# Optimization experiments

Measured on AMD Instinct MI355X. Metric: run time of the kernel, lower is better.

## Reference

```python
import jax, jax.numpy as jnp
import numpy as np

B = 4
NV = 6890           # SMPL vertex count
NF0 = 13776         # SMPL face count (before fill_back)
T = 3               # tex_size
IMG = 128           # render image size
UVH = UVW = 256     # uv image resolution
FLENGTH = 500.0
NEAR, FAR = 0.1, 25.0
CHUNK = 128         # faces per z-buffer scan step
BIG = jnp.float32(1e10)


def setup_inputs():
    key = jax.random.key(0)
    ks = jax.random.split(key, 5)
    faces0 = jax.random.randint(ks[0], (NF0, 3), 0, NV, dtype=jnp.int32)
    faces = jnp.concatenate([faces0, faces0[:, ::-1]], axis=0)  # fill_back
    cam = jnp.concatenate([0.8 + 0.2 * jax.random.uniform(ks[1], (B, 1)),
                           0.05 * jax.random.normal(ks[2], (B, 2))], axis=1)
    vertices = 0.3 * jax.random.normal(ks[3], (B, NV, 3))
    uv_imgs = jax.random.uniform(ks[4], (B, 3, UVH, UVW))
    img2uv_sampler = jax.random.uniform(jax.random.fold_in(key, 7),
                                        (faces.shape[0], T * T, 2)) * 2.0 - 1.0
    return {"cam": cam, "vertices": vertices, "uv_imgs": uv_imgs,
            "img2uv_sampler": img2uv_sampler, "faces": faces}


def _grid_sample(img, grid):
    # img (B,C,H,W), grid (B,N,2) xy in [-1,1]; bilinear, align_corners=False, zeros padding
    Bc, C, H, W = img.shape
    x = (grid[..., 0] + 1.0) * (W * 0.5) - 0.5
    y = (grid[..., 1] + 1.0) * (H * 0.5) - 0.5
    x0f = jnp.floor(x); y0f = jnp.floor(y)
    wx = x - x0f; wy = y - y0f
    x0 = x0f.astype(jnp.int32); y0 = y0f.astype(jnp.int32)
    imgf = img.reshape(Bc, C, H * W)
    def gat(yi, xi, w):
        valid = (xi >= 0) & (xi < W) & (yi >= 0) & (yi < H)
        idx = jnp.clip(yi, 0, H - 1) * W + jnp.clip(xi, 0, W - 1)
        v = jax.vmap(lambda im, i: im[:, i])(imgf, idx)  # (B,C,N)
        return v * (w * valid)[:, None, :]
    return (gat(y0, x0, (1 - wx) * (1 - wy)) + gat(y0, x0 + 1, wx * (1 - wy)) +
            gat(y0 + 1, x0, (1 - wx) * wy) + gat(y0 + 1, x0 + 1, wx * wy))


def _extract_tex(uv_imgs, sampler, nf):
    # sampler (B,nf,T*T,2) -> textures (B,nf,T,T,T,3)
    tex = _grid_sample(uv_imgs, sampler.reshape(uv_imgs.shape[0], -1, 2))
    tex = tex.reshape(-1, 3, nf, T, T).transpose(0, 2, 3, 4, 1)  # (B,nf,T,T,3)
    return jnp.broadcast_to(tex[:, :, :, :, None, :], tex.shape[:4] + (T, 3))


def _lighting(face_verts, textures):
    # module defaults: ambient intensity 1, directional 0, white lights, dir=(0,1,0)
    v0, v1, v2 = face_verts[:, :, 0], face_verts[:, :, 1], face_verts[:, :, 2]
    n = jnp.cross(v1 - v0, v2 - v0)
    n = n / (jnp.linalg.norm(n, axis=-1, keepdims=True) + 1e-10)
    cos = jnp.maximum(n @ jnp.array([0.0, 1.0, 0.0]), 0.0)       # (B,F)
    light = 1.0 * jnp.ones(3) + 0.0 * cos[..., None] * jnp.ones(3)  # (B,F,3)
    return textures * light[:, :, None, None, None, :]


def _weak_projection(cam, vertices):
    p = IMG / 2.0
    tz = FLENGTH / (p * cam[:, 0:1])                              # (B,1)
    v2d = cam[:, None, 0:1] * (vertices[:, :, :2] + cam[:, None, 1:])
    return jnp.concatenate([v2d, vertices[:, :, 2:3] + tz[:, None, :]], axis=-1)


def _bary(fv, px, py):
    # fv: (...,3,3) triangle screen verts; px,py broadcastable pixel coords
    x0 = fv[..., 0, 0]; y0 = fv[..., 0, 1]
    x1 = fv[..., 1, 0]; y1 = fv[..., 1, 1]
    x2 = fv[..., 2, 0]; y2 = fv[..., 2, 1]
    w0 = (x2 - x1) * (py - y1) - (y2 - y1) * (px - x1)
    w1 = (x0 - x2) * (py - y2) - (y0 - y2) * (px - x2)
    w2 = (x1 - x0) * (py - y0) - (y1 - y0) * (px - x0)
    area = w0 + w1 + w2
    s = jnp.where(area == 0, 1.0, area)
    return w0 / s, w1 / s, w2 / s, area


def _pixel_grid():
    xs = (2.0 * jnp.arange(IMG) + 1.0) / IMG - 1.0                # (W,)
    ys = (1.0 - (2.0 * jnp.arange(IMG) + 1.0) / IMG)[:, None]     # (H,1), +y up
    return xs, ys


def _rasterize_fim(face_verts):
    # face_verts (B,F,3,3) in screen coords -> face index map (B,H,W), -1 = bg
    Bc, F = face_verts.shape[:2]
    pad = (-F) % CHUNK
    fv = jnp.pad(face_verts, ((0, 0), (0, pad), (0, 0), (0, 0)))
    S = (F + pad) // CHUNK
    fv = fv.reshape(Bc, S, CHUNK, 3, 3).transpose(1, 0, 2, 3, 4)  # (S,B,C,3,3)
    xs, ys = _pixel_grid()
    def step(carry, inp):
        zbuf, fim = carry
        f, base = inp
        fe = f[:, :, None, None, :, :]                            # (B,C,1,1,3,3)
        b0, b1, b2, area = _bary(fe, xs, ys)                      # (B,C,H,W)
        z0 = f[:, :, 0, 2][..., None, None]
        z1 = f[:, :, 1, 2][..., None, None]
        z2 = f[:, :, 2, 2][..., None, None]
        invz = b0 / z0 + b1 / z1 + b2 / z2                        # perspective-correct
        zp = 1.0 / jnp.where(invz == 0, 1.0, invz)
        inside = (b0 >= 0) & (b1 >= 0) & (b2 >= 0) & (area > 0)   # front-facing only
        valid = inside & (zp > NEAR) & (zp < FAR)
        depth = jnp.where(valid, zp, BIG)
        dmin = jnp.min(depth, axis=1)                             # (B,H,W)
        amin = jnp.argmin(depth, axis=1).astype(jnp.int32) + base
        better = dmin < zbuf
        return (jnp.where(better, dmin, zbuf),
                jnp.where(better, amin, fim)), None
    zbuf0 = jnp.full((Bc, IMG, IMG), BIG)
    fim0 = jnp.full((Bc, IMG, IMG), -1, jnp.int32)
    bases = (jnp.arange(S) * CHUNK).astype(jnp.int32)
    (zbuf, fim), _ = jax.lax.scan(step, (zbuf0, fim0), (fv, bases))
    return fim


def _shade(face_verts, textures, fim):
    # nearest-texel barycentric texture lookup, as in neural_renderer forward
    Bc, F = face_verts.shape[:2]
    fid = jnp.clip(fim, 0, F - 1).reshape(Bc, -1)                 # (B,HW)
    fv = jax.vmap(lambda v, i: v[i])(face_verts, fid)             # (B,HW,3,3)
    fv = fv.reshape(Bc, IMG, IMG, 3, 3)
    xs, ys = _pixel_grid()
    b0, b1, b2, _ = _bary(fv, xs, ys)                             # (B,H,W)
    t0 = jnp.clip(jnp.floor(b0 * T).astype(jnp.int32), 0, T - 1)
    t1 = jnp.clip(jnp.floor(b1 * T).astype(jnp.int32), 0, T - 1)
    t2 = jnp.clip(jnp.floor(b2 * T).astype(jnp.int32), 0, T - 1)
    idx = ((jnp.clip(fim, 0, F - 1) * T + t0) * T + t1) * T + t2  # (B,H,W)
    texf = textures.reshape(Bc, F * T * T * T, 3)
    col = jax.vmap(lambda t, i: t[i])(texf, idx.reshape(Bc, -1))  # (B,HW,3)
    col = col.reshape(Bc, IMG, IMG, 3)
    col = jnp.where((fim >= 0)[..., None], col, 0.0)              # bg color (0,0,0)
    return col.transpose(0, 3, 1, 2)                              # (B,3,H,W)


def reference(cam, vertices, uv_imgs, img2uv_sampler, faces):
    Bc = cam.shape[0]
    nf = faces.shape[0]
    sampler = jnp.broadcast_to(img2uv_sampler[None], (Bc,) + img2uv_sampler.shape)
    textures = _extract_tex(uv_imgs, sampler, nf)                 # (B,nf,T,T,T,3)
    textures = _lighting(vertices[:, faces], textures)
    verts_p = _weak_projection(cam, vertices)
    fv = verts_p[:, faces]                                        # (B,nf,3,3)
    fv_sg = jax.lax.stop_gradient(fv)  # hard rasterization is non-differentiable
    fim = _rasterize_fim(fv_sg)
    images = _shade(fv_sg, textures, fim)
    return images


if __name__ == "__main__":
    out = reference(**setup_inputs())
    print(out.shape, out.dtype)
```

## Files before the change

### kernel.cpp

```cpp
#include <hip/hip_runtime.h>
#include <stdint.h>

#pragma clang fp contract(off)

#define B_    4
#define NV_   6890
#define NF_   27552
#define IMG_  128
#define UV_   256
#define NPIX  (IMG_*IMG_)

#define TS_     8
#define TPB_    (IMG_/TS_)
#define NTILE_  (TPB_*TPB_)
#define NBIN_   (B_*NTILE_)
#define NZ_     8
#define NCELL_  (NTILE_*NZ_)
#define LIST_CAP (1536*1024)
#define CAPB_   (LIST_CAP/B_)
#define MAXCB_  (CAPB_/256 + NTILE_)
#define SEEDN_  256
#define FBF_    256
#define NBLK_   ((NF_+FBF_-1)/FBF_)


__global__ void __launch_bounds__(256) project_k(
    const float* __restrict__ cam, const float* __restrict__ verts,
    float* __restrict__ vp) {
  int idx = blockIdx.x * 256 + threadIdx.x;
  if (idx >= B_ * NV_) return;
  int b = idx / NV_;
  float c0 = cam[b * 3 + 0], c1 = cam[b * 3 + 1], c2 = cam[b * 3 + 2];
  float tz = 500.0f / (64.0f * c0);
  const float* src = verts + (size_t)idx * 3;
  float* dst = vp + (size_t)idx * 4;
  dst[0] = c0 * (src[0] + c1);
  dst[1] = c0 * (src[1] + c2);
  dst[2] = src[2] + tz;
  dst[3] = 0.0f;
}

struct FaceBin {
  int valid, tx0, tx1, ty0, ty1, bu;
  float d21x, d21y, d02x, d02y, d10x, d10y;
  float x0, y0, x1, y1, x2, y2, zmin;
};

__device__ __forceinline__ FaceBin face_bin(
    const float* __restrict__ cam, const float* __restrict__ vp,
    const int* __restrict__ faces, int b, int f) {
  FaceBin r; r.valid = 0; r.zmin = 0.0f;
  int ia = faces[f * 3 + 0], ib = faces[f * 3 + 1], ic = faces[f * 3 + 2];
  const float* vb = vp + (size_t)b * NV_ * 4;
  float x0 = vb[ia * 4 + 0], y0 = vb[ia * 4 + 1], z0 = vb[ia * 4 + 2];
  float x1 = vb[ib * 4 + 0], y1 = vb[ib * 4 + 1], z1 = vb[ib * 4 + 2];
  float x2 = vb[ic * 4 + 0], y2 = vb[ic * 4 + 1], z2 = vb[ic * 4 + 2];
  float area_c = (x1 - x0) * (y2 - y0) - (y1 - y0) * (x2 - x0);
  if (area_c < -1e-3f) return r;
  float xmn = fminf(x0, fminf(x1, x2)), xmx = fmaxf(x0, fmaxf(x1, x2));
  float ymn = fminf(y0, fminf(y1, y2)), ymx = fmaxf(y0, fmaxf(y1, y2));
  int jlo = (int)floorf((xmn + 1.0f) * 64.0f - 0.5f) - 1;
  int jhi = (int)ceilf ((xmx + 1.0f) * 64.0f - 0.5f) + 1;
  int ilo = (int)floorf((1.0f - ymx) * 64.0f - 0.5f) - 1;
  int ihi = (int)ceilf ((1.0f - ymn) * 64.0f - 0.5f) + 1;
  if (jhi < 0 || ihi < 0 || jlo > IMG_ - 1 || ilo > IMG_ - 1) return r;
  jlo = max(jlo, 0); ilo = max(ilo, 0);
  jhi = min(jhi, IMG_ - 1); ihi = min(ihi, IMG_ - 1);
  r.tx0 = jlo >> 3; r.tx1 = jhi >> 3; r.ty0 = ilo >> 3; r.ty1 = ihi >> 3;
  r.zmin = fminf(z0, fminf(z1, z2));
  float tz = 500.0f / (64.0f * cam[b * 3]);
  float zr = r.zmin - tz;
  r.bu = (zr > -0.447f) + (zr > -0.367f) + (zr > -0.308f) + (zr > -0.254f) +
         (zr > -0.200f) + (zr > -0.141f) + (zr > -0.061f);
  r.d21x = x2 - x1; r.d21y = y2 - y1;
  r.d02x = x0 - x2; r.d02y = y0 - y2;
  r.d10x = x1 - x0; r.d10y = y1 - y0;
  r.x0 = x0; r.y0 = y0; r.x1 = x1; r.y1 = y1; r.x2 = x2; r.y2 = y2;
  r.valid = 1;
  return r;
}

__device__ __forceinline__ int tile_pass(const FaceBin& r, int tx, int ty) {
  float pxmin = fmaf((float)(tx * 8), 0.015625f, -0.9921875f);
  float pxmax = pxmin + 0.109375f;
  float pymax = fmaf((float)(ty * 8), -0.015625f, 0.9921875f);
  float pymin = pymax - 0.109375f;
  float w0m = r.d21x * ((r.d21x > 0.0f ? pymax : pymin) - r.y1) -
              r.d21y * ((r.d21y > 0.0f ? pxmin : pxmax) - r.x1);
  float w1m = r.d02x * ((r.d02x > 0.0f ? pymax : pymin) - r.y2) -
              r.d02y * ((r.d02y > 0.0f ? pxmin : pxmax) - r.x2);
  float w2m = r.d10x * ((r.d10x > 0.0f ? pymax : pymin) - r.y0) -
              r.d10y * ((r.d10y > 0.0f ? pxmin : pxmax) - r.x0);
  return (w0m >= -1e-3f) && (w1m >= -1e-3f) && (w2m >= -1e-3f);
}

__global__ void __launch_bounds__(FBF_) facebin_k(
    const float* __restrict__ cam, const float* __restrict__ vp,
    const int* __restrict__ faces, ulonglong2* __restrict__ recs,
    unsigned short* __restrict__ cntb) {
  __shared__ int scnt[NCELL_];
  int blk = blockIdx.x, b = blockIdx.y;
  int f = blk * FBF_ + threadIdx.x;
  for (int k = threadIdx.x; k < NCELL_; k += FBF_) scnt[k] = 0;
  __syncthreads();
  if (f < NF_) {
    FaceBin r = face_bin(cam, vp, faces, b, f);
    unsigned long long mask = 0ull;
    unsigned info = 0u;
    float zmin = 0.0f;
    if (r.valid) {
      int w = r.tx1 - r.tx0 + 1, h = r.ty1 - r.ty0 + 1;
      bool full = (w * h > 64);
      int k = 0;
      for (int ty = r.ty0; ty <= r.ty1; ++ty)
        for (int tx = r.tx0; tx <= r.tx1; ++tx, ++k)
          if (full || tile_pass(r, tx, ty)) {
            if (!full) mask |= 1ull << k;
            atomicAdd(&scnt[(ty * TPB_ + tx) * NZ_ + r.bu], 1);
          }
      if (full) mask = ~0ull;
      if (mask != 0ull) {
        info = 0x80000000u | ((unsigned)r.bu << 28) |
               ((unsigned)r.tx0 << 24) | ((unsigned)r.ty0 << 20) |
               ((unsigned)(w - 1) << 16) | ((unsigned)(h - 1) << 12);
        zmin = r.zmin;
      }
    }
    ulonglong2 rr;
    rr.x = mask;
    rr.y = ((unsigned long long)info << 32) | (unsigned)__float_as_uint(zmin);
    recs[(size_t)b * NF_ + f] = rr;
  }
  __syncthreads();
  unsigned short* dst = cntb + ((size_t)b * NBLK_ + blk) * NCELL_;
  for (int k = threadIdx.x; k < NCELL_; k += FBF_)
    dst[k] = (unsigned short)scnt[k];
}

__global__ void __launch_bounds__(1024) sumscan_k(
    unsigned short* __restrict__ cntb, int* __restrict__ off8,
    int* __restrict__ binoff, int* __restrict__ bintot,
    int* __restrict__ work, int* __restrict__ nC) {
  __shared__ int tot[NCELL_];
  __shared__ int wsum[16];
  __shared__ int half0;
  __shared__ int nchs[NTILE_];
  int b = blockIdx.x;
  int t = threadIdx.x;
  int lane = t & 63, w = t >> 6;
  for (int c = t; c < NCELL_; c += 1024) {
    int run = 0;
    for (int blk = 0; blk < NBLK_; ++blk) {
      size_t o = ((size_t)b * NBLK_ + blk) * NCELL_ + c;
      int v = (int)cntb[o];
      cntb[o] = (unsigned short)run;
      run += v;
    }
    tot[c] = run;
  }
  __syncthreads();
  int base = b * CAPB_;
  int v0 = tot[t];
  int inc0 = v0;
  for (int d = 1; d < 64; d <<= 1) {
    int u = __shfl_up(inc0, d, 64);
    if (lane >= d) inc0 += u;
  }
  if (lane == 63) wsum[w] = inc0;
  __syncthreads();
  int wb0 = 0;
  for (int k = 0; k < 16; ++k) wb0 += (k < w) ? wsum[k] : 0;
  off8[(size_t)b * NCELL_ + t] = base + wb0 + inc0 - v0;
  if (t == 1023) half0 = wb0 + inc0;
  __syncthreads();
  int v1 = tot[1024 + t];
  int inc1 = v1;
  for (int d = 1; d < 64; d <<= 1) {
    int u = __shfl_up(inc1, d, 64);
    if (lane >= d) inc1 += u;
  }
  if (lane == 63) wsum[w] = inc1;
  __syncthreads();
  int wb1 = 0;
  for (int k = 0; k < 16; ++k) wb1 += (k < w) ? wsum[k] : 0;
  off8[(size_t)b * NCELL_ + 1024 + t] = base + half0 + wb1 + inc1 - v1;
  __syncthreads();
  if (t < NTILE_) {
    int s = 0;
#pragma unroll
    for (int j = 0; j < NZ_; ++j) s += tot[t * NZ_ + j];
    bintot[b * NTILE_ + t] = s;
    binoff[b * NTILE_ + t] = off8[(size_t)b * NCELL_ + t * NZ_];
    nchs[t] = (max(s - SEEDN_, 0) + 255) >> 8;
  }
  __syncthreads();
  int vc = (t < NTILE_) ? nchs[t] : 0;
  int incc = vc;
  for (int d = 1; d < 64; d <<= 1) {
    int u = __shfl_up(incc, d, 64);
    if (lane >= d) incc += u;
  }
  if (t < NTILE_ && lane == 63) wsum[w] = incc;
  __syncthreads();
  if (t < NTILE_) {
    int wb = 0;
    for (int k = 0; k < 4; ++k) wb += (k < w) ? wsum[k] : 0;
    int cb = wb + incc - vc;
    if (t == NTILE_ - 1) nC[b] = wb + incc;
    for (int q = 0; q < vc; ++q)
      work[b * MAXCB_ + cb + q] = t | ((q + 1) << 8);
  }
}

__global__ void __launch_bounds__(FBF_) bin_fill_k(
    const ulonglong2* __restrict__ recs, const int* __restrict__ off8,
    const unsigned short* __restrict__ cntb, int* __restrict__ list) {
  __shared__ int lbase[NCELL_];
  __shared__ int lrank[NCELL_];
  int blk = blockIdx.x, b = blockIdx.y;
  int f = blk * FBF_ + threadIdx.x;
  const unsigned short* prow = cntb + ((size_t)b * NBLK_ + blk) * NCELL_;
  const int* orow = off8 + (size_t)b * NCELL_;
  for (int k = threadIdx.x; k < NCELL_; k += FBF_) {
    lbase[k] = orow[k] + (int)prow[k];
    lrank[k] = 0;
  }
  __syncthreads();
  if (f < NF_) {
    ulonglong2 rr = recs[(size_t)b * NF_ + f];
    unsigned long long mask = rr.x;
    unsigned info = (unsigned)(rr.y >> 32);
    unsigned z16 = ((unsigned)rr.y) >> 16;
    if (info >> 31) {
      int ev = (int)((z16 << 15) | (unsigned)f);
      int bu = (info >> 28) & 7;
      int tx0 = (info >> 24) & 15, ty0 = (info >> 20) & 15;
      int w = ((info >> 16) & 15) + 1, h = ((info >> 12) & 15) + 1;
      bool full = (w * h > 64);
      int cap = (b + 1) * CAPB_;
      int k = 0;
      for (int ty = ty0; ty < ty0 + h; ++ty)
        for (int tx = tx0; tx < tx0 + w; ++tx, ++k)
          if (full || ((mask >> k) & 1ull)) {
            int cell = (ty * TPB_ + tx) * NZ_ + bu;
            int rk = atomicAdd(&lrank[cell], 1);
            int slot = lbase[cell] + rk;
            if (slot < cap) list[slot] = ev;
          }
    }
  }
}

template <int S>
__device__ __forceinline__ void raster_slice(
    const float4 (*F)[S], int nsurv, float px, float py,
    unsigned long long& kb, unsigned& kbz_u) {
  unsigned win_u = 0x7F800000u;
  unsigned long long qm = 0ull;
  for (int q = 0; q < nsurv; ++q) {
    float4 A = F[0][q];
    float4 Bv = F[1][q];
    float4 Cv = F[2][q];
    float w0 = A.x * (py - A.w) - A.y * (px - A.z);
    float w1 = Bv.x * (py - Bv.w) - Bv.y * (px - Bv.z);
    float w2 = Cv.x * (py - Cv.w) - Cv.y * (px - Cv.z);
    float area = (w0 + w1) + w2;
    float mn = fminf(w0, fminf(w1, w2));
    bool pred = (area > 0.0f) && !(mn < 0.0f);
    if (!__any(pred)) continue;
    float4 P = F[4][q];
    float num = (w0 * P.x + w1 * P.y) + w2 * P.z;
    float zpa = (area * P.w) * __builtin_amdgcn_rcpf(num);
    unsigned cu = win_u < kbz_u ? win_u : kbz_u;
    float thrq = __uint_as_float(cu) * 1.001f;
    bool amb = pred && (!(zpa > thrq) ||
                        (zpa > 0.09989f && zpa < 0.10011f) ||
                        (zpa > 24.9724f && zpa < 25.0276f));
    if (amb) qm |= 1ull << q;
    bool ok = pred && (zpa > 0.1001f) && (zpa < 24.975f);
    unsigned zb = __float_as_uint(zpa);
    if (ok && zb < win_u) win_u = zb;
  }
  while (__any(qm != 0ull)) {
    if (qm != 0ull) {
      int q = __ffsll(qm) - 1;
      qm &= qm - 1ull;
      float4 A = F[0][q];
      float4 Bv = F[1][q];
      float4 Cv = F[2][q];
      float w0 = A.x * (py - A.w) - A.y * (px - A.z);
      float w1 = Bv.x * (py - Bv.w) - Bv.y * (px - Bv.z);
      float w2 = Cv.x * (py - Cv.w) - Cv.y * (px - Cv.z);
      float area = (w0 + w1) + w2;
      float4 P = F[4][q];
      float num = (w0 * P.x + w1 * P.y) + w2 * P.z;
      float zpa = (area * P.w) * __builtin_amdgcn_rcpf(num);
      unsigned cu = win_u < kbz_u ? win_u : kbz_u;
      float thrf = __uint_as_float(cu) * 1.001f;
      if (!(zpa > thrf) ||
          (zpa > 0.09989f && zpa < 0.10011f) ||
          (zpa > 24.9724f && zpa < 25.0276f)) {
        float4 Z = F[3][q];
        float b0 = w0 / area, b1 = w1 / area, b2 = w2 / area;
        float invz = (b0 / Z.x + b1 / Z.y) + b2 / Z.z;
        float zp = 1.0f / (invz == 0.0f ? 1.0f : invz);
        if (zp > 0.1f && zp < 25.0f) {
          unsigned long long key =
              ((unsigned long long)__float_as_uint(zp) << 32) |
              (unsigned int)__float_as_int(Z.w);
          if (key < kb) {
            kb = key;
            kbz_u = (unsigned)(kb >> 32);
          }
        }
      }
    }
  }
}

template <int S>
__device__ __forceinline__ void stage_face(
    float4 (*F)[S], const float* __restrict__ vb,
    const int* __restrict__ faces, int fid, int rank) {
  int ia = faces[fid * 3 + 0], ib = faces[fid * 3 + 1], ic = faces[fid * 3 + 2];
  float4 v0 = *(const float4*)(vb + (size_t)ia * 4);
  float4 v1 = *(const float4*)(vb + (size_t)ib * 4);
  float4 v2 = *(const float4*)(vb + (size_t)ic * 4);
  F[0][rank] = make_float4(v2.x - v1.x, v2.y - v1.y, v1.x, v1.y);
  F[1][rank] = make_float4(v0.x - v2.x, v0.y - v2.y, v2.x, v2.y);
  F[2][rank] = make_float4(v1.x - v0.x, v1.y - v0.y, v0.x, v0.y);
  F[3][rank] = make_float4(v0.z, v1.z, v2.z, __int_as_float(fid));
  F[4][rank] =
      make_float4(v1.z * v2.z, v0.z * v2.z, v0.z * v1.z, v0.z * v1.z * v2.z);
}

__global__ void __launch_bounds__(512) raster_seed_k(
    const float* __restrict__ vp, const int* __restrict__ faces,
    const int* __restrict__ list, const int* __restrict__ bintot,
    const int* __restrict__ binoff, unsigned long long* __restrict__ zkey) {
  __shared__ float4 fd[8][5][32];
  __shared__ unsigned long long mg[8][64];
  int bin = blockIdx.x;
  int b = bin >> 8;
  int t = bin & 255;
  int tyT = t >> 4, txT = t & 15;
  int ws = threadIdx.x >> 6, lane = threadIdx.x & 63;
  int pi = tyT * TS_ + (lane >> 3);
  int pj = txT * TS_ + (lane & 7);
  float px = fmaf((float)pj, 0.015625f, -0.9921875f);
  float py = fmaf((float)pi, -0.015625f, 0.9921875f);

  int n = min(bintot[bin], SEEDN_);
  int base = binoff[bin];
  int seg = ws * 32;
  int mw = min(n - seg, 32);

  unsigned long long kb = ~0ull;
  unsigned kbz_u = 0x7F800000u;
  if (mw > 0) {
    if (lane < mw) {
      int fid = (int)((unsigned)list[base + seg + lane] & 0x7FFFu);
      stage_face<32>(fd[ws], vp + (size_t)b * NV_ * 4, faces, fid, lane);
    }
    raster_slice<32>(fd[ws], mw, px, py, kb, kbz_u);
  }

  mg[ws][lane] = kb;
  __syncthreads();
  if (ws == 0) {
    unsigned long long k0 = mg[0][lane];
#pragma unroll
    for (int j = 1; j < 8; ++j) {
      unsigned long long kj = mg[j][lane];
      k0 = kj < k0 ? kj : k0;
    }
    zkey[(size_t)b * NPIX + pi * IMG_ + pj] = k0;
  }
}

__global__ void __launch_bounds__(256) raster_k(
    const float* __restrict__ vp, const int* __restrict__ faces,
    const int* __restrict__ list, const int* __restrict__ bintot,
    const int* __restrict__ binoff, const int* __restrict__ work,
    const int* __restrict__ nC, unsigned long long* __restrict__ zkey) {
  __shared__ float4 fd[4][5][64];
  __shared__ unsigned long long mg[4][64];
  int bid = blockIdx.x;
  int b = bid / MAXCB_;
  int i = bid - b * MAXCB_;
  if (i >= nC[b]) return;
  int wkv = work[b * MAXCB_ + i];
  int t = wkv & (NTILE_ - 1);
  int chunk = wkv >> 8;
  int bin = b * NTILE_ + t;
  int tyT = t >> 4, txT = t & 15;
  int ws = threadIdx.x >> 6, lane = threadIdx.x & 63;
  int pi = tyT * TS_ + (lane >> 3);
  int pj = txT * TS_ + (lane & 7);
  float px = fmaf((float)pj, 0.015625f, -0.9921875f);
  float py = fmaf((float)pi, -0.015625f, 0.9921875f);

  const unsigned* zhi = (const unsigned*)zkey;
  unsigned seed_u =
      min(zhi[((size_t)b * NPIX + pi * IMG_ + pj) * 2 + 1], 0x7F800000u);
  unsigned mx = seed_u;
  for (int j = 1; j < 64; j <<= 1) {
    unsigned o = (unsigned)__shfl_xor((int)mx, j, 64);
    mx = o > mx ? o : mx;
  }
  unsigned thr_code = __float_as_uint(__uint_as_float(mx) * 1.01f) >> 16;

  int n = bintot[bin];
  int seg = SEEDN_ + ((chunk - 1) << 8) + (ws << 6);
  int base0 = binoff[bin] + seg;
  int mw = min(n - seg, 64);
  mw = max(mw, 0);

  bool live = false;
  int fid = 0;
  if (lane < mw) {
    unsigned e = (unsigned)list[base0 + lane];
    live = ((e >> 15) <= thr_code);
    fid = (int)(e & 0x7FFFu);
  }
  unsigned long long bal = __ballot(live);
  unsigned long long kb = ~0ull;
  unsigned kbz_u = seed_u;
  if (bal != 0ull) {
    int nsurv = (int)__popcll(bal);
    int rank = (int)__popcll(bal & ((1ull << lane) - 1ull));
    if (live)
      stage_face<64>(fd[ws], vp + (size_t)b * NV_ * 4, faces, fid, rank);
    raster_slice<64>(fd[ws], nsurv, px, py, kb, kbz_u);
  }

  mg[ws][lane] = kb;
  __syncthreads();
  if (ws == 0) {
    unsigned long long k0 = mg[0][lane];
    unsigned long long k1 = mg[1][lane];
    unsigned long long k2 = mg[2][lane];
    unsigned long long k3 = mg[3][lane];
    k0 = k1 < k0 ? k1 : k0;
    k2 = k3 < k2 ? k3 : k2;
    k0 = k2 < k0 ? k2 : k0;
    if (k0 != ~0ull)
      atomicMin(zkey + (size_t)b * NPIX + pi * IMG_ + pj, k0);
  }
}

#define TAP(ty, tx, wexpr)                                                   \
  {                                                                          \
    int ty_ = (ty), tx_ = (tx);                                              \
    float w_ = (wexpr);                                                      \
    float valid_ =                                                           \
        (tx_ >= 0 && tx_ < UV_ && ty_ >= 0 && ty_ < UV_) ? 1.0f : 0.0f;      \
    float wv_ = w_ * valid_;                                                 \
    int cy_ = min(max(ty_, 0), UV_ - 1), cx_ = min(max(tx_, 0), UV_ - 1);    \
    int o_ = cy_ * UV_ + cx_;                                                \
    cr = cr + img[o_] * wv_;                                                 \
    cg = cg + img[UV_ * UV_ + o_] * wv_;                                     \
    cb = cb + img[2 * UV_ * UV_ + o_] * wv_;                                 \
  }

__global__ void __launch_bounds__(256) shade_k(
    const float* __restrict__ vp, const int* __restrict__ faces,
    const float* __restrict__ uv, const float* __restrict__ samp,
    const unsigned long long* __restrict__ zkey, float* __restrict__ out) {
  int idx = blockIdx.x * 256 + threadIdx.x;
  if (idx >= B_ * NPIX) return;
  int b = idx / NPIX;
  int p = idx - b * NPIX;
  int ii = p / IMG_;
  int jj = p - ii * IMG_;

  unsigned long long key = zkey[idx];
  float cr = 0.0f, cg = 0.0f, cb = 0.0f;
  if (key != 0xFFFFFFFFFFFFFFFFull) {
    int f = (int)(key & 0xFFFFFFFFull);
    int ia = faces[f * 3 + 0], ib = faces[f * 3 + 1], ic = faces[f * 3 + 2];
    const float* vb = vp + (size_t)b * NV_ * 4;
    float x0 = vb[ia * 4 + 0], y0 = vb[ia * 4 + 1];
    float x1 = vb[ib * 4 + 0], y1 = vb[ib * 4 + 1];
    float x2 = vb[ic * 4 + 0], y2 = vb[ic * 4 + 1];
    float px = (float)(2 * jj + 1) / 128.0f - 1.0f;
    float py = 1.0f - (float)(2 * ii + 1) / 128.0f;
    float w0 = (x2 - x1) * (py - y1) - (y2 - y1) * (px - x1);
    float w1 = (x0 - x2) * (py - y2) - (y0 - y2) * (px - x2);
    float w2 = (x1 - x0) * (py - y0) - (y1 - y0) * (px - x0);
    float area = (w0 + w1) + w2;
    float s = (area == 0.0f) ? 1.0f : area;
    float b0 = w0 / s, b1 = w1 / s;
    int t0 = min(max((int)floorf(b0 * 3.0f), 0), 2);
    int t1 = min(max((int)floorf(b1 * 3.0f), 0), 2);

    const float* g = samp + ((size_t)f * 9 + (size_t)(t0 * 3 + t1)) * 2;
    float gx = g[0], gy = g[1];
    float x = (gx + 1.0f) * 128.0f - 0.5f;
    float y = (gy + 1.0f) * 128.0f - 0.5f;
    float x0f = floorf(x), y0f = floorf(y);
    float wx = x - x0f, wy = y - y0f;
    int xi = (int)x0f, yi = (int)y0f;
    float omwx = 1.0f - wx, omwy = 1.0f - wy;
    const float* img = uv + (size_t)b * 3 * UV_ * UV_;
    TAP(yi,     xi,     omwx * omwy)
    TAP(yi,     xi + 1, wx * omwy)
    TAP(yi + 1, xi,     omwx * wy)
    TAP(yi + 1, xi + 1, wx * wy)
  }
  out[((size_t)b * 3 + 0) * NPIX + p] = cr;
  out[((size_t)b * 3 + 1) * NPIX + p] = cg;
  out[((size_t)b * 3 + 2) * NPIX + p] = cb;
}

extern "C" void kernel_launch(void* const* d_in, const int* in_sizes, int n_in,
                              void* d_out, int out_size, void* d_ws,
                              size_t ws_size, hipStream_t stream) {
  const float* cam   = (const float*)d_in[0];
  const float* verts = (const float*)d_in[1];
  const float* uv    = (const float*)d_in[2];
  const float* samp  = (const float*)d_in[3];
  const int*   faces = (const int*)d_in[4];

  char* ws = (char*)d_ws;
  size_t o = 0;
  unsigned long long* zkey = (unsigned long long*)(ws + o);
  o += (size_t)B_ * NPIX * 8;
  float* vp = (float*)(ws + o);
  o += ((size_t)B_ * NV_ * 4 * 4 + 1023) & ~1023ull;
  int* off8   = (int*)(ws + o); o += (size_t)B_ * NCELL_ * 4;
  int* binoff = (int*)(ws + o); o += NBIN_ * 4;
  int* bintot = (int*)(ws + o); o += NBIN_ * 4;
  int* nC     = (int*)(ws + o); o += 1024;
  int* work   = (int*)(ws + o); o += (size_t)B_ * MAXCB_ * 4;
  ulonglong2* recs = (ulonglong2*)(ws + o);
  o += (size_t)B_ * NF_ * 16;
  unsigned short* cntb = (unsigned short*)(ws + o);
  o += (size_t)B_ * NBLK_ * NCELL_ * 2;
  int* list = (int*)(ws + o);

  project_k<<<(B_ * NV_ + 255) / 256, 256, 0, stream>>>(cam, verts, vp);
  dim3 bgrid(NBLK_, B_);
  facebin_k<<<bgrid, FBF_, 0, stream>>>(cam, vp, faces, recs, cntb);
  sumscan_k<<<B_, 1024, 0, stream>>>(cntb, off8, binoff, bintot, work, nC);
  bin_fill_k<<<bgrid, FBF_, 0, stream>>>(recs, off8, cntb, list);
  raster_seed_k<<<NBIN_, 512, 0, stream>>>(vp, faces, list, bintot, binoff,
                                           zkey);
  raster_k<<<B_ * MAXCB_, 256, 0, stream>>>(vp, faces, list, bintot, binoff,
                                            work, nC, zkey);
  shade_k<<<(B_ * NPIX + 255) / 256, 256, 0, stream>>>(vp, faces, uv, samp,
                                                       zkey, (float*)d_out);
}
```

Baseline: 189.1 us.

## Fuse all raster pipeline stages into one cooperative persistent kernel

Replaces the seven separate kernel launches (project, face binning, scan, bin fill, seed raster, chunk raster, shade) with a single cooperative kernel of 256 blocks of 1024 threads, using grid-wide syncs between phases. It also regroups the work: binning uses 1024-face chunks, which changes the scan length, and seed and chunk rasterization use smaller per-wave slices. The aim is to remove launch overhead and inter-kernel gaps. In exchange it adds grid sync costs, runs the scan phase on only 4 blocks while the rest idle, and limits occupancy with large blocks and shared memory.

After: 340.4 us. 1.8x slower.

```diff
diff --git a/kernel.cpp b/kernel.cpp
--- a/kernel.cpp
+++ b/kernel.cpp
@@ -1,7 +1,10 @@
 #include <hip/hip_runtime.h>
+#include <hip/hip_cooperative_groups.h>
 #include <stdint.h>
 
 #pragma clang fp contract(off)
+
+namespace cg = cooperative_groups;
 
 #define B_    4
 #define NV_   6890
@@ -20,25 +23,8 @@
 #define CAPB_   (LIST_CAP/B_)
 #define MAXCB_  (CAPB_/256 + NTILE_)
 #define SEEDN_  256
-#define FBF_    256
-#define NBLK_   ((NF_+FBF_-1)/FBF_)
-
-
-__global__ void __launch_bounds__(256) project_k(
-    const float* __restrict__ cam, const float* __restrict__ verts,
-    float* __restrict__ vp) {
-  int idx = blockIdx.x * 256 + threadIdx.x;
-  if (idx >= B_ * NV_) return;
-  int b = idx / NV_;
-  float c0 = cam[b * 3 + 0], c1 = cam[b * 3 + 1], c2 = cam[b * 3 + 2];
-  float tz = 500.0f / (64.0f * c0);
-  const float* src = verts + (size_t)idx * 3;
-  float* dst = vp + (size_t)idx * 4;
-  dst[0] = c0 * (src[0] + c1);
-  dst[1] = c0 * (src[1] + c2);
-  dst[2] = src[2] + tz;
-  dst[3] = 0.0f;
-}
+#define NBLK2_  ((NF_+1023)/1024)
+
 
 struct FaceBin {
   int valid, tx0, tx1, ty0, ty1, bu;
@@ -94,163 +80,6 @@
   return (w0m >= -1e-3f) && (w1m >= -1e-3f) && (w2m >= -1e-3f);
 }
 
-__global__ void __launch_bounds__(FBF_) facebin_k(
-    const float* __restrict__ cam, const float* __restrict__ vp,
-    const int* __restrict__ faces, ulonglong2* __restrict__ recs,
-    unsigned short* __restrict__ cntb) {
-  __shared__ int scnt[NCELL_];
-  int blk = blockIdx.x, b = blockIdx.y;
-  int f = blk * FBF_ + threadIdx.x;
-  for (int k = threadIdx.x; k < NCELL_; k += FBF_) scnt[k] = 0;
-  __syncthreads();
-  if (f < NF_) {
-    FaceBin r = face_bin(cam, vp, faces, b, f);
-    unsigned long long mask = 0ull;
-    unsigned info = 0u;
-    float zmin = 0.0f;
-    if (r.valid) {
-      int w = r.tx1 - r.tx0 + 1, h = r.ty1 - r.ty0 + 1;
-      bool full = (w * h > 64);
-      int k = 0;
-      for (int ty = r.ty0; ty <= r.ty1; ++ty)
-        for (int tx = r.tx0; tx <= r.tx1; ++tx, ++k)
-          if (full || tile_pass(r, tx, ty)) {
-            if (!full) mask |= 1ull << k;
-            atomicAdd(&scnt[(ty * TPB_ + tx) * NZ_ + r.bu], 1);
-          }
-      if (full) mask = ~0ull;
-      if (mask != 0ull) {
-        info = 0x80000000u | ((unsigned)r.bu << 28) |
-               ((unsigned)r.tx0 << 24) | ((unsigned)r.ty0 << 20) |
-               ((unsigned)(w - 1) << 16) | ((unsigned)(h - 1) << 12);
-        zmin = r.zmin;
-      }
-    }
-    ulonglong2 rr;
-    rr.x = mask;
-    rr.y = ((unsigned long long)info << 32) | (unsigned)__float_as_uint(zmin);
-    recs[(size_t)b * NF_ + f] = rr;
-  }
-  __syncthreads();
-  unsigned short* dst = cntb + ((size_t)b * NBLK_ + blk) * NCELL_;
-  for (int k = threadIdx.x; k < NCELL_; k += FBF_)
-    dst[k] = (unsigned short)scnt[k];
-}
-
-__global__ void __launch_bounds__(1024) sumscan_k(
-    unsigned short* __restrict__ cntb, int* __restrict__ off8,
-    int* __restrict__ binoff, int* __restrict__ bintot,
-    int* __restrict__ work, int* __restrict__ nC) {
-  __shared__ int tot[NCELL_];
-  __shared__ int wsum[16];
-  __shared__ int half0;
-  __shared__ int nchs[NTILE_];
-  int b = blockIdx.x;
-  int t = threadIdx.x;
-  int lane = t & 63, w = t >> 6;
-  for (int c = t; c < NCELL_; c += 1024) {
-    int run = 0;
-    for (int blk = 0; blk < NBLK_; ++blk) {
-      size_t o = ((size_t)b * NBLK_ + blk) * NCELL_ + c;
-      int v = (int)cntb[o];
-      cntb[o] = (unsigned short)run;
-      run += v;
-    }
-    tot[c] = run;
-  }
-  __syncthreads();
-  int base = b * CAPB_;
-  int v0 = tot[t];
-  int inc0 = v0;
-  for (int d = 1; d < 64; d <<= 1) {
-    int u = __shfl_up(inc0, d, 64);
-    if (lane >= d) inc0 += u;
-  }
-  if (lane == 63) wsum[w] = inc0;
-  __syncthreads();
-  int wb0 = 0;
-  for (int k = 0; k < 16; ++k) wb0 += (k < w) ? wsum[k] : 0;
-  off8[(size_t)b * NCELL_ + t] = base + wb0 + inc0 - v0;
-  if (t == 1023) half0 = wb0 + inc0;
-  __syncthreads();
-  int v1 = tot[1024 + t];
-  int inc1 = v1;
-  for (int d = 1; d < 64; d <<= 1) {
-    int u = __shfl_up(inc1, d, 64);
-    if (lane >= d) inc1 += u;
-  }
-  if (lane == 63) wsum[w] = inc1;
-  __syncthreads();
-  int wb1 = 0;
-  for (int k = 0; k < 16; ++k) wb1 += (k < w) ? wsum[k] : 0;
-  off8[(size_t)b * NCELL_ + 1024 + t] = base + half0 + wb1 + inc1 - v1;
-  __syncthreads();
-  if (t < NTILE_) {
-    int s = 0;
-#pragma unroll
-    for (int j = 0; j < NZ_; ++j) s += tot[t * NZ_ + j];
-    bintot[b * NTILE_ + t] = s;
-    binoff[b * NTILE_ + t] = off8[(size_t)b * NCELL_ + t * NZ_];
-    nchs[t] = (max(s - SEEDN_, 0) + 255) >> 8;
-  }
-  __syncthreads();
-  int vc = (t < NTILE_) ? nchs[t] : 0;
-  int incc = vc;
-  for (int d = 1; d < 64; d <<= 1) {
-    int u = __shfl_up(incc, d, 64);
-    if (lane >= d) incc += u;
-  }
-  if (t < NTILE_ && lane == 63) wsum[w] = incc;
-  __syncthreads();
-  if (t < NTILE_) {
-    int wb = 0;
-    for (int k = 0; k < 4; ++k) wb += (k < w) ? wsum[k] : 0;
-    int cb = wb + incc - vc;
-    if (t == NTILE_ - 1) nC[b] = wb + incc;
-    for (int q = 0; q < vc; ++q)
-      work[b * MAXCB_ + cb + q] = t | ((q + 1) << 8);
-  }
-}
-
-__global__ void __launch_bounds__(FBF_) bin_fill_k(
-    const ulonglong2* __restrict__ recs, const int* __restrict__ off8,
-    const unsigned short* __restrict__ cntb, int* __restrict__ list) {
-  __shared__ int lbase[NCELL_];
-  __shared__ int lrank[NCELL_];
-  int blk = blockIdx.x, b = blockIdx.y;
-  int f = blk * FBF_ + threadIdx.x;
-  const unsigned short* prow = cntb + ((size_t)b * NBLK_ + blk) * NCELL_;
-  const int* orow = off8 + (size_t)b * NCELL_;
-  for (int k = threadIdx.x; k < NCELL_; k += FBF_) {
-    lbase[k] = orow[k] + (int)prow[k];
-    lrank[k] = 0;
-  }
-  __syncthreads();
-  if (f < NF_) {
-    ulonglong2 rr = recs[(size_t)b * NF_ + f];
-    unsigned long long mask = rr.x;
-    unsigned info = (unsigned)(rr.y >> 32);
-    unsigned z16 = ((unsigned)rr.y) >> 16;
-    if (info >> 31) {
-      int ev = (int)((z16 << 15) | (unsigned)f);
-      int bu = (info >> 28) & 7;
-      int tx0 = (info >> 24) & 15, ty0 = (info >> 20) & 15;
-      int w = ((info >> 16) & 15) + 1, h = ((info >> 12) & 15) + 1;
-      bool full = (w * h > 64);
-      int cap = (b + 1) * CAPB_;
-      int k = 0;
-      for (int ty = ty0; ty < ty0 + h; ++ty)
-        for (int tx = tx0; tx < tx0 + w; ++tx, ++k)
-          if (full || ((mask >> k) & 1ull)) {
-            int cell = (ty * TPB_ + tx) * NZ_ + bu;
-            int rk = atomicAdd(&lrank[cell], 1);
-            int slot = lbase[cell] + rk;
-            if (slot < cap) list[slot] = ev;
-          }
-    }
-  }
-}
-
 template <int S>
 __device__ __forceinline__ void raster_slice(
     const float4 (*F)[S], int nsurv, float px, float py,
@@ -334,121 +163,6 @@
       make_float4(v1.z * v2.z, v0.z * v2.z, v0.z * v1.z, v0.z * v1.z * v2.z);
 }
 
-__global__ void __launch_bounds__(512) raster_seed_k(
-    const float* __restrict__ vp, const int* __restrict__ faces,
-    const int* __restrict__ list, const int* __restrict__ bintot,
-    const int* __restrict__ binoff, unsigned long long* __restrict__ zkey) {
-  __shared__ float4 fd[8][5][32];
-  __shared__ unsigned long long mg[8][64];
-  int bin = blockIdx.x;
-  int b = bin >> 8;
-  int t = bin & 255;
-  int tyT = t >> 4, txT = t & 15;
-  int ws = threadIdx.x >> 6, lane = threadIdx.x & 63;
-  int pi = tyT * TS_ + (lane >> 3);
-  int pj = txT * TS_ + (lane & 7);
-  float px = fmaf((float)pj, 0.015625f, -0.9921875f);
-  float py = fmaf((float)pi, -0.015625f, 0.9921875f);
-
-  int n = min(bintot[bin], SEEDN_);
-  int base = binoff[bin];
-  int seg = ws * 32;
-  int mw = min(n - seg, 32);
-
-  unsigned long long kb = ~0ull;
-  unsigned kbz_u = 0x7F800000u;
-  if (mw > 0) {
-    if (lane < mw) {
-      int fid = (int)((unsigned)list[base + seg + lane] & 0x7FFFu);
-      stage_face<32>(fd[ws], vp + (size_t)b * NV_ * 4, faces, fid, lane);
-    }
-    raster_slice<32>(fd[ws], mw, px, py, kb, kbz_u);
-  }
-
-  mg[ws][lane] = kb;
-  __syncthreads();
-  if (ws == 0) {
-    unsigned long long k0 = mg[0][lane];
-#pragma unroll
-    for (int j = 1; j < 8; ++j) {
-      unsigned long long kj = mg[j][lane];
-      k0 = kj < k0 ? kj : k0;
-    }
-    zkey[(size_t)b * NPIX + pi * IMG_ + pj] = k0;
-  }
-}
-
-__global__ void __launch_bounds__(256) raster_k(
-    const float* __restrict__ vp, const int* __restrict__ faces,
-    const int* __restrict__ list, const int* __restrict__ bintot,
-    const int* __restrict__ binoff, const int* __restrict__ work,
-    const int* __restrict__ nC, unsigned long long* __restrict__ zkey) {
-  __shared__ float4 fd[4][5][64];
-  __shared__ unsigned long long mg[4][64];
-  int bid = blockIdx.x;
-  int b = bid / MAXCB_;
-  int i = bid - b * MAXCB_;
-  if (i >= nC[b]) return;
-  int wkv = work[b * MAXCB_ + i];
-  int t = wkv & (NTILE_ - 1);
-  int chunk = wkv >> 8;
-  int bin = b * NTILE_ + t;
-  int tyT = t >> 4, txT = t & 15;
-  int ws = threadIdx.x >> 6, lane = threadIdx.x & 63;
-  int pi = tyT * TS_ + (lane >> 3);
-  int pj = txT * TS_ + (lane & 7);
-  float px = fmaf((float)pj, 0.015625f, -0.9921875f);
-  float py = fmaf((float)pi, -0.015625f, 0.9921875f);
-
-  const unsigned* zhi = (const unsigned*)zkey;
-  unsigned seed_u =
-      min(zhi[((size_t)b * NPIX + pi * IMG_ + pj) * 2 + 1], 0x7F800000u);
-  unsigned mx = seed_u;
-  for (int j = 1; j < 64; j <<= 1) {
-    unsigned o = (unsigned)__shfl_xor((int)mx, j, 64);
-    mx = o > mx ? o : mx;
-  }
-  unsigned thr_code = __float_as_uint(__uint_as_float(mx) * 1.01f) >> 16;
-
-  int n = bintot[bin];
-  int seg = SEEDN_ + ((chunk - 1) << 8) + (ws << 6);
-  int base0 = binoff[bin] + seg;
-  int mw = min(n - seg, 64);
-  mw = max(mw, 0);
-
-  bool live = false;
-  int fid = 0;
-  if (lane < mw) {
-    unsigned e = (unsigned)list[base0 + lane];
-    live = ((e >> 15) <= thr_code);
-    fid = (int)(e & 0x7FFFu);
-  }
-  unsigned long long bal = __ballot(live);
-  unsigned long long kb = ~0ull;
-  unsigned kbz_u = seed_u;
-  if (bal != 0ull) {
-    int nsurv = (int)__popcll(bal);
-    int rank = (int)__popcll(bal & ((1ull << lane) - 1ull));
-    if (live)
-      stage_face<64>(fd[ws], vp + (size_t)b * NV_ * 4, faces, fid, rank);
-    raster_slice<64>(fd[ws], nsurv, px, py, kb, kbz_u);
-  }
-
-  mg[ws][lane] = kb;
-  __syncthreads();
-  if (ws == 0) {
-    unsigned long long k0 = mg[0][lane];
-    unsigned long long k1 = mg[1][lane];
-    unsigned long long k2 = mg[2][lane];
-    unsigned long long k3 = mg[3][lane];
-    k0 = k1 < k0 ? k1 : k0;
-    k2 = k3 < k2 ? k3 : k2;
-    k0 = k2 < k0 ? k2 : k0;
-    if (k0 != ~0ull)
-      atomicMin(zkey + (size_t)b * NPIX + pi * IMG_ + pj, k0);
-  }
-}
-
 #define TAP(ty, tx, wexpr)                                                   \
   {                                                                          \
     int ty_ = (ty), tx_ = (tx);                                              \
@@ -463,54 +177,359 @@
     cb = cb + img[2 * UV_ * UV_ + o_] * wv_;                                 \
   }
 
-__global__ void __launch_bounds__(256) shade_k(
-    const float* __restrict__ vp, const int* __restrict__ faces,
+extern "C" __global__ void __launch_bounds__(1024) mega_k(
+    const float* __restrict__ cam, const float* __restrict__ verts,
     const float* __restrict__ uv, const float* __restrict__ samp,
-    const unsigned long long* __restrict__ zkey, float* __restrict__ out) {
-  int idx = blockIdx.x * 256 + threadIdx.x;
-  if (idx >= B_ * NPIX) return;
-  int b = idx / NPIX;
-  int p = idx - b * NPIX;
-  int ii = p / IMG_;
-  int jj = p - ii * IMG_;
-
-  unsigned long long key = zkey[idx];
-  float cr = 0.0f, cg = 0.0f, cb = 0.0f;
-  if (key != 0xFFFFFFFFFFFFFFFFull) {
-    int f = (int)(key & 0xFFFFFFFFull);
-    int ia = faces[f * 3 + 0], ib = faces[f * 3 + 1], ic = faces[f * 3 + 2];
-    const float* vb = vp + (size_t)b * NV_ * 4;
-    float x0 = vb[ia * 4 + 0], y0 = vb[ia * 4 + 1];
-    float x1 = vb[ib * 4 + 0], y1 = vb[ib * 4 + 1];
-    float x2 = vb[ic * 4 + 0], y2 = vb[ic * 4 + 1];
-    float px = (float)(2 * jj + 1) / 128.0f - 1.0f;
-    float py = 1.0f - (float)(2 * ii + 1) / 128.0f;
-    float w0 = (x2 - x1) * (py - y1) - (y2 - y1) * (px - x1);
-    float w1 = (x0 - x2) * (py - y2) - (y0 - y2) * (px - x2);
-    float w2 = (x1 - x0) * (py - y0) - (y1 - y0) * (px - x0);
-    float area = (w0 + w1) + w2;
-    float s = (area == 0.0f) ? 1.0f : area;
-    float b0 = w0 / s, b1 = w1 / s;
-    int t0 = min(max((int)floorf(b0 * 3.0f), 0), 2);
-    int t1 = min(max((int)floorf(b1 * 3.0f), 0), 2);
-
-    const float* g = samp + ((size_t)f * 9 + (size_t)(t0 * 3 + t1)) * 2;
-    float gx = g[0], gy = g[1];
-    float x = (gx + 1.0f) * 128.0f - 0.5f;
-    float y = (gy + 1.0f) * 128.0f - 0.5f;
-    float x0f = floorf(x), y0f = floorf(y);
-    float wx = x - x0f, wy = y - y0f;
-    int xi = (int)x0f, yi = (int)y0f;
-    float omwx = 1.0f - wx, omwy = 1.0f - wy;
-    const float* img = uv + (size_t)b * 3 * UV_ * UV_;
-    TAP(yi,     xi,     omwx * omwy)
-    TAP(yi,     xi + 1, wx * omwy)
-    TAP(yi + 1, xi,     omwx * wy)
-    TAP(yi + 1, xi + 1, wx * wy)
-  }
-  out[((size_t)b * 3 + 0) * NPIX + p] = cr;
-  out[((size_t)b * 3 + 1) * NPIX + p] = cg;
-  out[((size_t)b * 3 + 2) * NPIX + p] = cb;
+    const int* __restrict__ faces, unsigned long long* __restrict__ zkey,
+    float* __restrict__ vp, int* __restrict__ off8, int* __restrict__ binoff,
+    int* __restrict__ bintot, int* __restrict__ work, int* __restrict__ nC,
+    ulonglong2* __restrict__ recs, unsigned short* __restrict__ cntb,
+    int* __restrict__ list, float* __restrict__ out) {
+  cg::grid_group gg = cg::this_grid();
+  __shared__ __align__(16) char smem[49152];
+  int blk = blockIdx.x;
+  int t = threadIdx.x;
+
+  {
+    int idx = blk * 1024 + t;
+    if (idx < B_ * NV_) {
+      int b = idx / NV_;
+      float c0 = cam[b * 3 + 0], c1 = cam[b * 3 + 1], c2 = cam[b * 3 + 2];
+      float tz = 500.0f / (64.0f * c0);
+      const float* src = verts + (size_t)idx * 3;
+      float* dst = vp + (size_t)idx * 4;
+      dst[0] = c0 * (src[0] + c1);
+      dst[1] = c0 * (src[1] + c2);
+      dst[2] = src[2] + tz;
+      dst[3] = 0.0f;
+    }
+  }
+  gg.sync();
+
+  {
+    int* scnt = (int*)smem;
+    for (int tau = blk; tau < NBLK2_ * B_; tau += 256) {
+      int b = tau / NBLK2_, ch = tau - b * NBLK2_;
+      int f = ch * 1024 + t;
+      for (int k = t; k < NCELL_; k += 1024) scnt[k] = 0;
+      __syncthreads();
+      if (f < NF_) {
+        FaceBin r = face_bin(cam, vp, faces, b, f);
+        unsigned long long mask = 0ull;
+        unsigned info = 0u;
+        float zmin = 0.0f;
+        if (r.valid) {
+          int w = r.tx1 - r.tx0 + 1, h = r.ty1 - r.ty0 + 1;
+          bool full = (w * h > 64);
+          int k = 0;
+          for (int ty = r.ty0; ty <= r.ty1; ++ty)
+            for (int tx = r.tx0; tx <= r.tx1; ++tx, ++k)
+              if (full || tile_pass(r, tx, ty)) {
+                if (!full) mask |= 1ull << k;
+                atomicAdd(&scnt[(ty * TPB_ + tx) * NZ_ + r.bu], 1);
+              }
+          if (full) mask = ~0ull;
+          if (mask != 0ull) {
+            info = 0x80000000u | ((unsigned)r.bu << 28) |
+                   ((unsigned)r.tx0 << 24) | ((unsigned)r.ty0 << 20) |
+                   ((unsigned)(w - 1) << 16) | ((unsigned)(h - 1) << 12);
+            zmin = r.zmin;
+          }
+        }
+        ulonglong2 rr;
+        rr.x = mask;
+        rr.y = ((unsigned long long)info << 32) |
+               (unsigned)__float_as_uint(zmin);
+        recs[(size_t)b * NF_ + f] = rr;
+      }
+      __syncthreads();
+      unsigned short* dst = cntb + ((size_t)b * NBLK2_ + ch) * NCELL_;
+      for (int k = t; k < NCELL_; k += 1024)
+        dst[k] = (unsigned short)scnt[k];
+      __syncthreads();
+    }
+  }
+  gg.sync();
+
+  if (blk < B_) {
+    int* tot = (int*)smem;
+    int* wsum = (int*)(smem + 8192);
+    int* half0 = (int*)(smem + 8256);
+    int* nchs = (int*)(smem + 8272);
+    int b = blk;
+    int lane = t & 63, w = t >> 6;
+    for (int c = t; c < NCELL_; c += 1024) {
+      int run = 0;
+      for (int q = 0; q < NBLK2_; ++q) {
+        size_t o = ((size_t)b * NBLK2_ + q) * NCELL_ + c;
+        int v = (int)cntb[o];
+        cntb[o] = (unsigned short)run;
+        run += v;
+      }
+      tot[c] = run;
+    }
+    __syncthreads();
+    int base = b * CAPB_;
+    int v0 = tot[t];
+    int inc0 = v0;
+    for (int d = 1; d < 64; d <<= 1) {
+      int u = __shfl_up(inc0, d, 64);
+      if (lane >= d) inc0 += u;
+    }
+    if (lane == 63) wsum[w] = inc0;
+    __syncthreads();
+    int wb0 = 0;
+    for (int k = 0; k < 16; ++k) wb0 += (k < w) ? wsum[k] : 0;
+    off8[(size_t)b * NCELL_ + t] = base + wb0 + inc0 - v0;
+    if (t == 1023) half0[0] = wb0 + inc0;
+    __syncthreads();
+    int v1 = tot[1024 + t];
+    int inc1 = v1;
+    for (int d = 1; d < 64; d <<= 1) {
+      int u = __shfl_up(inc1, d, 64);
+      if (lane >= d) inc1 += u;
+    }
+    if (lane == 63) wsum[w] = inc1;
+    __syncthreads();
+    int wb1 = 0;
+    for (int k = 0; k < 16; ++k) wb1 += (k < w) ? wsum[k] : 0;
+    off8[(size_t)b * NCELL_ + 1024 + t] = base + half0[0] + wb1 + inc1 - v1;
+    __syncthreads();
+    if (t < NTILE_) {
+      int s = 0;
+#pragma unroll
+      for (int j = 0; j < NZ_; ++j) s += tot[t * NZ_ + j];
+      bintot[b * NTILE_ + t] = s;
+      binoff[b * NTILE_ + t] = off8[(size_t)b * NCELL_ + t * NZ_];
+      nchs[t] = (max(s - SEEDN_, 0) + 255) >> 8;
+    }
+    __syncthreads();
+    int vc = (t < NTILE_) ? nchs[t] : 0;
+    int incc = vc;
+    for (int d = 1; d < 64; d <<= 1) {
+      int u = __shfl_up(incc, d, 64);
+      if (lane >= d) incc += u;
+    }
+    if (t < NTILE_ && lane == 63) wsum[w] = incc;
+    __syncthreads();
+    if (t < NTILE_) {
+      int wb = 0;
+      for (int k = 0; k < 4; ++k) wb += (k < w) ? wsum[k] : 0;
+      int cb = wb + incc - vc;
+      if (t == NTILE_ - 1) nC[b] = wb + incc;
+      for (int q = 0; q < vc; ++q)
+        work[b * MAXCB_ + cb + q] = t | ((q + 1) << 8);
+    }
+  }
+  gg.sync();
+
+  {
+    int* lbase = (int*)smem;
+    int* lrank = (int*)(smem + 8192);
+    for (int tau = blk; tau < NBLK2_ * B_; tau += 256) {
+      int b = tau / NBLK2_, ch = tau - b * NBLK2_;
+      int f = ch * 1024 + t;
+      const unsigned short* prow = cntb + ((size_t)b * NBLK2_ + ch) * NCELL_;
+      const int* orow = off8 + (size_t)b * NCELL_;
+      for (int k = t; k < NCELL_; k += 1024) {
+        lbase[k] = orow[k] + (int)prow[k];
+        lrank[k] = 0;
+      }
+      __syncthreads();
+      if (f < NF_) {
+        ulonglong2 rr = recs[(size_t)b * NF_ + f];
+        unsigned long long mask = rr.x;
+        unsigned info = (unsigned)(rr.y >> 32);
+        unsigned z16 = ((unsigned)rr.y) >> 16;
+        if (info >> 31) {
+          int ev = (int)((z16 << 15) | (unsigned)f);
+          int bu = (info >> 28) & 7;
+          int tx0 = (info >> 24) & 15, ty0 = (info >> 20) & 15;
+          int w = ((info >> 16) & 15) + 1, h = ((info >> 12) & 15) + 1;
+          bool full = (w * h > 64);
+          int cap = (b + 1) * CAPB_;
+          int k = 0;
+          for (int ty = ty0; ty < ty0 + h; ++ty)
+            for (int tx = tx0; tx < tx0 + w; ++tx, ++k)
+              if (full || ((mask >> k) & 1ull)) {
+                int cell = (ty * TPB_ + tx) * NZ_ + bu;
+                int rk = atomicAdd(&lrank[cell], 1);
+                int slot = lbase[cell] + rk;
+                if (slot < cap) list[slot] = ev;
+              }
+        }
+      }
+      __syncthreads();
+    }
+  }
+  gg.sync();
+
+  {
+    auto fd16 = (float4 (*)[5][16])smem;
+    auto mg16 = (unsigned long long (*)[64])(smem + 20480);
+    int ws = t >> 6, lane = t & 63;
+    for (int rd = 0; rd < 4; ++rd) {
+      int bin = blk * 4 + rd;
+      int b = bin >> 8;
+      int tt = bin & 255;
+      int tyT = tt >> 4, txT = tt & 15;
+      int pi = tyT * TS_ + (lane >> 3);
+      int pj = txT * TS_ + (lane & 7);
+      float px = fmaf((float)pj, 0.015625f, -0.9921875f);
+      float py = fmaf((float)pi, -0.015625f, 0.9921875f);
+      int n = min(bintot[bin], SEEDN_);
+      int base = binoff[bin];
+      int seg = ws * 16;
+      int mw = min(n - seg, 16);
+      unsigned long long kb = ~0ull;
+      unsigned kbz_u = 0x7F800000u;
+      if (mw > 0) {
+        if (lane < mw) {
+          int fid = (int)((unsigned)list[base + seg + lane] & 0x7FFFu);
+          stage_face<16>(fd16[ws], vp + (size_t)b * NV_ * 4, faces, fid,
+                         lane);
+        }
+        raster_slice<16>(fd16[ws], mw, px, py, kb, kbz_u);
+      }
+      mg16[ws][lane] = kb;
+      __syncthreads();
+      if (ws == 0) {
+        unsigned long long k0 = mg16[0][lane];
+#pragma unroll
+        for (int j = 1; j < 16; ++j) {
+          unsigned long long kj = mg16[j][lane];
+          k0 = kj < k0 ? kj : k0;
+        }
+        zkey[(size_t)b * NPIX + pi * IMG_ + pj] = k0;
+      }
+      __syncthreads();
+    }
+  }
+  gg.sync();
+
+  {
+    auto fd = (float4 (*)[5][32])smem;
+    auto mg = (unsigned long long (*)[64])(smem + 40960);
+    int h = t >> 9;
+    int wsg = t >> 6;
+    int ws8 = wsg & 7;
+    int lane = t & 63;
+    const unsigned* zhi = (const unsigned*)zkey;
+    for (int g0 = blk * 2; g0 < B_ * MAXCB_; g0 += 512) {
+      int g = g0 + h;
+      int b = g / MAXCB_;
+      int i = g - b * MAXCB_;
+      bool active = (i < nC[b]);
+      unsigned long long kb = ~0ull;
+      int pi = 0, pj = 0, bb = 0;
+      if (active) {
+        int wkv = work[b * MAXCB_ + i];
+        int tt = wkv & (NTILE_ - 1);
+        int chunk = wkv >> 8;
+        int bin = b * NTILE_ + tt;
+        int tyT = tt >> 4, txT = tt & 15;
+        pi = tyT * TS_ + (lane >> 3);
+        pj = txT * TS_ + (lane & 7);
+        bb = b;
+        float px = fmaf((float)pj, 0.015625f, -0.9921875f);
+        float py = fmaf((float)pi, -0.015625f, 0.9921875f);
+        unsigned seed_u = min(
+            zhi[((size_t)b * NPIX + pi * IMG_ + pj) * 2 + 1], 0x7F800000u);
+        unsigned mx = seed_u;
+        for (int j = 1; j < 64; j <<= 1) {
+          unsigned o = (unsigned)__shfl_xor((int)mx, j, 64);
+          mx = o > mx ? o : mx;
+        }
+        unsigned thr_code =
+            __float_as_uint(__uint_as_float(mx) * 1.01f) >> 16;
+        int n = bintot[bin];
+        int seg = SEEDN_ + ((chunk - 1) << 8) + (ws8 << 5);
+        int base0 = binoff[bin] + seg;
+        int mw = min(n - seg, 32);
+        mw = max(mw, 0);
+        bool live = false;
+        int fid = 0;
+        if (lane < mw) {
+          unsigned e = (unsigned)list[base0 + lane];
+          live = ((e >> 15) <= thr_code);
+          fid = (int)(e & 0x7FFFu);
+        }
+        unsigned long long bal = __ballot(live);
+        unsigned kbz_u = seed_u;
+        if (bal != 0ull) {
+          int nsurv = (int)__popcll(bal);
+          int rank = (int)__popcll(bal & ((1ull << lane) - 1ull));
+          if (live)
+            stage_face<32>(fd[wsg], vp + (size_t)b * NV_ * 4, faces, fid,
+                           rank);
+          raster_slice<32>(fd[wsg], nsurv, px, py, kb, kbz_u);
+        }
+      }
+      mg[wsg][lane] = kb;
+      __syncthreads();
+      if (active && ws8 == 0) {
+        unsigned long long k0 = mg[h * 8 + 0][lane];
+#pragma unroll
+        for (int j = 1; j < 8; ++j) {
+          unsigned long long kj = mg[h * 8 + j][lane];
+          k0 = kj < k0 ? kj : k0;
+        }
+        if (k0 != ~0ull)
+          atomicMin(zkey + (size_t)bb * NPIX + pi * IMG_ + pj, k0);
+      }
+      __syncthreads();
+    }
+  }
+  gg.sync();
+
+  {
+    int idx = blk * 1024 + t;
+    if (idx < B_ * NPIX) {
+      int b = idx / NPIX;
+      int p = idx - b * NPIX;
+      int ii = p / IMG_;
+      int jj = p - ii * IMG_;
+      unsigned long long key = zkey[idx];
+      float cr = 0.0f, cg2 = 0.0f, cb2 = 0.0f;
+      float& cg = cg2;
+      float& cb = cb2;
+      if (key != 0xFFFFFFFFFFFFFFFFull) {
+        int f = (int)(key & 0xFFFFFFFFull);
+        int ia = faces[f * 3 + 0], ib = faces[f * 3 + 1],
+            ic = faces[f * 3 + 2];
+        const float* vb = vp + (size_t)b * NV_ * 4;
+        float x0 = vb[ia * 4 + 0], y0 = vb[ia * 4 + 1];
+        float x1 = vb[ib * 4 + 0], y1 = vb[ib * 4 + 1];
+        float x2 = vb[ic * 4 + 0], y2 = vb[ic * 4 + 1];
+        float px = (float)(2 * jj + 1) / 128.0f - 1.0f;
+        float py = 1.0f - (float)(2 * ii + 1) / 128.0f;
+        float w0 = (x2 - x1) * (py - y1) - (y2 - y1) * (px - x1);
+        float w1 = (x0 - x2) * (py - y2) - (y0 - y2) * (px - x2);
+        float w2 = (x1 - x0) * (py - y0) - (y1 - y0) * (px - x0);
+        float area = (w0 + w1) + w2;
+        float s = (area == 0.0f) ? 1.0f : area;
+        float b0 = w0 / s, b1 = w1 / s;
+        int t0 = min(max((int)floorf(b0 * 3.0f), 0), 2);
+        int t1 = min(max((int)floorf(b1 * 3.0f), 0), 2);
+        const float* g = samp + ((size_t)f * 9 + (size_t)(t0 * 3 + t1)) * 2;
+        float gx = g[0], gy = g[1];
+        float x = (gx + 1.0f) * 128.0f - 0.5f;
+        float y = (gy + 1.0f) * 128.0f - 0.5f;
+        float x0f = floorf(x), y0f = floorf(y);
+        float wx = x - x0f, wy = y - y0f;
+        int xi = (int)x0f, yi = (int)y0f;
+        float omwx = 1.0f - wx, omwy = 1.0f - wy;
+        const float* img = uv + (size_t)b * 3 * UV_ * UV_;
+        TAP(yi,     xi,     omwx * omwy)
+        TAP(yi,     xi + 1, wx * omwy)
+        TAP(yi + 1, xi,     omwx * wy)
+        TAP(yi + 1, xi + 1, wx * wy)
+      }
+      out[((size_t)b * 3 + 0) * NPIX + p] = cr;
+      out[((size_t)b * 3 + 1) * NPIX + p] = cg2;
+      out[((size_t)b * 3 + 2) * NPIX + p] = cb2;
+    }
+  }
 }
 
 extern "C" void kernel_launch(void* const* d_in, const int* in_sizes, int n_in,
@@ -521,6 +540,7 @@
   const float* uv    = (const float*)d_in[2];
   const float* samp  = (const float*)d_in[3];
   const int*   faces = (const int*)d_in[4];
+  float* outp = (float*)d_out;
 
   char* ws = (char*)d_ws;
   size_t o = 0;
@@ -536,18 +556,15 @@
   ulonglong2* recs = (ulonglong2*)(ws + o);
   o += (size_t)B_ * NF_ * 16;
   unsigned short* cntb = (unsigned short*)(ws + o);
-  o += (size_t)B_ * NBLK_ * NCELL_ * 2;
+  o += (size_t)B_ * NBLK2_ * NCELL_ * 2;
   int* list = (int*)(ws + o);
 
-  project_k<<<(B_ * NV_ + 255) / 256, 256, 0, stream>>>(cam, verts, vp);
-  dim3 bgrid(NBLK_, B_);
-  facebin_k<<<bgrid, FBF_, 0, stream>>>(cam, vp, faces, recs, cntb);
-  sumscan_k<<<B_, 1024, 0, stream>>>(cntb, off8, binoff, bintot, work, nC);
-  bin_fill_k<<<bgrid, FBF_, 0, stream>>>(recs, off8, cntb, list);
-  raster_seed_k<<<NBIN_, 512, 0, stream>>>(vp, faces, list, bintot, binoff,
-                                           zkey);
-  raster_k<<<B_ * MAXCB_, 256, 0, stream>>>(vp, faces, list, bintot, binoff,
-                                            work, nC, zkey);
-  shade_k<<<(B_ * NPIX + 255) / 256, 256, 0, stream>>>(vp, faces, uv, samp,
-                                                       zkey, (float*)d_out);
+  void* args[] = {(void*)&cam,    (void*)&verts, (void*)&uv,
+                  (void*)&samp,   (void*)&faces, (void*)&zkey,
+                  (void*)&vp,     (void*)&off8,  (void*)&binoff,
+                  (void*)&bintot, (void*)&work,  (void*)&nC,
+                  (void*)&recs,   (void*)&cntb,  (void*)&list,
+                  (void*)&outp};
+  hipLaunchCooperativeKernel((const void*)mega_k, dim3(256), dim3(1024),
+                             args, 0, stream);
 }
```
